# Kernel optimization log

Measured on AMD Instinct MI355X. Metric: run time of the kernel, lower is better.

## Reference

```python
import jax, jax.numpy as jnp
import numpy as np

N_CHAINS = 4
CHAIN_LEN = 512
N = N_CHAINS * CHAIN_LEN          # 2048 residues
H = 128                           # h_channels
FC = 3                            # frame_channels
CIN = H + FC                      # fused sphere channels (131)
NH = 8                            # attention heads
VD = H // 4                       # attn value channels per head
NCOEF = 4                         # lmax=1 -> (lmax+1)^2 coefficients
KNN_K = 30
LR_K = 10
NEG = jnp.float32(-1e30)

BB_IDEAL = np.array([[-0.525, 1.363, 0.0], [0.0, 0.0, 0.0], [1.526, 0.0, 0.0]], np.float32)  # N, CA, C ideal coords


def _safe_norm(v, keepdims=False):
    return jnp.sqrt(jnp.sum(v * v, axis=-1, keepdims=keepdims) + 1e-12)


def _normalize(v):
    return v / _safe_norm(v, keepdims=True)


def _edge_rot_mat(vec):
    # deterministic orthonormal frame with first row along the edge direction
    x = _normalize(vec)
    ref = jnp.where(jnp.abs(x[..., :1]) > 0.99,
                    jnp.array([0.0, 1.0, 0.0], x.dtype),
                    jnp.array([1.0, 0.0, 0.0], x.dtype))
    z = _normalize(jnp.cross(x, ref))
    y = jnp.cross(z, x)
    return jnp.stack([x, y, z], axis=-2)          # [E,3,3]


def _rbf(d, d_min=0.0, d_max=20.0, n=16):
    mu = jnp.linspace(d_min, d_max, n)
    sigma = (d_max - d_min) / n
    return jnp.exp(-(((d[..., None] - mu) / sigma) ** 2))


def _relpos(edge_index, n=16):
    d = (edge_index[0] - edge_index[1]).astype(jnp.float32)
    freq = jnp.exp(jnp.arange(0, n, 2, dtype=jnp.float32) * (-np.log(10000.0) / n))
    ang = d[:, None] * freq
    return jnp.concatenate([jnp.cos(ang), jnp.sin(ang)], axis=-1)


def _quat_to_rot(q):
    w, x, y, z = q[..., 0], q[..., 1], q[..., 2], q[..., 3]
    r0 = jnp.stack([1 - 2 * (y * y + z * z), 2 * (x * y - w * z), 2 * (x * z + w * y)], -1)
    r1 = jnp.stack([2 * (x * y + w * z), 1 - 2 * (x * x + z * z), 2 * (y * z - w * x)], -1)
    r2 = jnp.stack([2 * (x * z - w * y), 2 * (y * z + w * x), 1 - 2 * (x * x + y * y)], -1)
    return jnp.stack([r0, r1, r2], -2)


def _build_edges(trans, batch, seq_local_edge_index):
    d2 = jnp.sum((trans[:, None] - trans[None]) ** 2, -1)   # [N,N]
    same = batch[:, None] == batch[None]
    eye = jnp.eye(N, dtype=bool)
    d2m = jnp.where(same & ~eye, d2, jnp.float32(1e30))
    _, knn_idx = jax.lax.top_k(-d2m, KNN_K)                 # kNN neighbors
    g = jax.random.gumbel(jax.random.key(42), d2m.shape)
    _, lr_idx = jax.lax.top_k(-1.5 * jnp.log(d2m) + g, LR_K)  # inv-cubic sampling p ~ d^-3
    src = jnp.concatenate([knn_idx.reshape(-1), lr_idx.reshape(-1), seq_local_edge_index[0]])
    dst = jnp.concatenate([jnp.repeat(jnp.arange(N), KNN_K), jnp.repeat(jnp.arange(N), LR_K), seq_local_edge_index[1]])
    return jnp.stack([src, dst])


def _forward(rots, trans, node_features, Wa1, ba1, Wa2, Wv, Wo, Wg, Wf1, Wf2, Wr1, br1, Wr2, br2, Wr3, br3, Wt, batch, x_mask, noising_mask, seq_local_edge_index):
    edge_index = _build_edges(trans, batch, seq_local_edge_index)
    src, dst = edge_index[0], edge_index[1]
    vec = trans[src] - trans[dst]
    dist = _safe_norm(vec)
    valid = jnp.isfinite(dist) & (dist > 1e-3)              # edge_select mask (kept static-shape)
    R = _edge_rot_mat(vec)                                  # [E,3,3] per-edge Wigner (l=1)
    ef = jnp.concatenate([_rbf(dist), _relpos(edge_index)], -1)  # [E,32]
    # fuse node embedding with backbone frame atoms and editability flag
    bb_atoms = jnp.einsum('nij,aj->nai', rots, jnp.asarray(BB_IDEAL)) + trans[:, None]  # [N,3atoms,3]
    fused = jnp.zeros((N, NCOEF, CIN), node_features.dtype)
    fused = fused.at[:, :, :H].set(node_features)
    fused = fused.at[:, 1:4, H:].set(jnp.swapaxes(bb_atoms, -1, -2))
    editable = noising_mask & (~x_mask)
    fused = fused.at[:, 0, -1].set(editable.astype(fused.dtype))
    # SO3-equivariant attention (TransBlockV2)
    x0 = fused[:, 0]                                        # invariant l=0 features [N,CIN]
    a_in = jnp.concatenate([x0[src], x0[dst], ef], -1)      # [E, 2*CIN+32]
    logits = jax.nn.leaky_relu(a_in @ Wa1 + ba1) @ Wa2      # [E,NH]
    logits = jnp.where(valid[:, None], logits, NEG)
    m = jax.ops.segment_max(logits, dst, num_segments=N)
    m = jnp.where(m > NEG / 2, m, 0.0)
    p = jnp.where(valid[:, None], jnp.exp(logits - m[dst]), 0.0)
    z = jax.ops.segment_sum(p, dst, num_segments=N)
    attn = p / (z[dst] + 1e-9)                              # segment softmax over incoming edges
    xs = fused[src]
    xs = xs.at[:, 1:4].set(jnp.einsum('eij,ejc->eic', R, xs[:, 1:4]))  # rotate l=1 into edge frame
    v = (xs @ Wv).reshape(xs.shape[0], NCOEF, NH, VD)
    msg = (attn[:, None, :, None] * v).reshape(xs.shape[0], NCOEF, NH * VD)
    msg = msg.at[:, 1:4].set(jnp.einsum('eji,ejc->eic', R, msg[:, 1:4]))  # rotate back (R^T)
    agg = jax.ops.segment_sum(msg, dst, num_segments=N)     # [N,4,NH*VD]
    out = agg @ Wo                                          # [N,4,H]
    # gated equivariant FFN
    y0 = out[:, 0]
    gate = jax.nn.sigmoid(y0 @ Wg)
    f0 = jax.nn.relu(y0 @ Wf1) @ Wf2
    bb_update = jnp.concatenate([(y0 + f0)[:, None], out[:, 1:4] * gate[:, None, :]], axis=1)
    # frame rotation update from invariants
    inv = bb_update[:, 0]
    h1 = jax.nn.relu(inv @ Wr1 + br1)
    h2 = jax.nn.relu(h1 @ Wr2 + br2)
    qv = (h2 @ Wr3 + br3)[:, :3]
    quat = jnp.concatenate([jnp.ones_like(qv[:, :1]), qv], -1)
    quat = quat / jnp.linalg.norm(quat, axis=-1, keepdims=True)
    rot_update = _quat_to_rot(quat)
    # equivariant translation update (SO3_LinearV2 on l=1)
    trans_update = (bb_update[:, 1:4] @ Wt)[..., 0]         # [N,3]
    rots_new = jnp.where(noising_mask[:, None, None], jnp.einsum('nij,njk->nik', rots, rot_update), rots)
    trans_new = jnp.where(noising_mask[:, None], trans + trans_update, trans)
    return rots_new, trans_new, bb_update


def setup_inputs():
    key = jax.random.key(0)
    ks = jax.random.split(key, 20)
    q = jax.random.normal(ks[0], (N, 4))
    q = q / jnp.linalg.norm(q, axis=-1, keepdims=True)
    rots = _quat_to_rot(q)                                  # proper rotation matrices
    trans = jax.random.normal(ks[1], (N, 3)) * 10.0
    node_features = jax.random.normal(ks[2], (N, NCOEF, H)) * 0.1
    batch = jnp.repeat(jnp.arange(N_CHAINS), CHAIN_LEN)
    x_mask = jax.random.bernoulli(ks[3], 0.1, (N,))
    noising_mask = jax.random.bernoulli(ks[4], 0.5, (N,))
    idx = jnp.arange(N)
    nxt = jnp.where((idx + 1) % CHAIN_LEN == 0, idx, idx + 1)
    seq_local_edge_index = jnp.stack([jnp.concatenate([idx, nxt]), jnp.concatenate([nxt, idx])])

    def lin(k, i, o):
        return jax.random.normal(k, (i, o)) / np.sqrt(i)

    AIN = 2 * CIN + 32
    return dict(
        rots=rots, trans=trans, node_features=node_features,
        Wa1=lin(ks[5], AIN, H), ba1=jnp.zeros((H,)),
        Wa2=lin(ks[6], H, NH),
        Wv=lin(ks[7], CIN, NH * VD),
        Wo=lin(ks[8], NH * VD, H),
        Wg=lin(ks[9], H, H), Wf1=lin(ks[10], H, H), Wf2=lin(ks[11], H, H),
        Wr1=lin(ks[12], H, 2 * H), br1=jnp.zeros((2 * H,)),
        Wr2=lin(ks[13], 2 * H, H), br2=jnp.zeros((H,)),
        Wr3=lin(ks[14], H, 6), br3=jnp.zeros((6,)),
        Wt=lin(ks[15], H, 1),
        batch=batch, x_mask=x_mask, noising_mask=noising_mask,
        seq_local_edge_index=seq_local_edge_index)


def reference(rots, trans, node_features, Wa1, ba1, Wa2, Wv, Wo, Wg, Wf1, Wf2, Wr1, br1, Wr2, br2, Wr3, br3, Wt, batch, x_mask, noising_mask, seq_local_edge_index):
    return _forward(rots, trans, node_features, Wa1, ba1, Wa2, Wv, Wo, Wg, Wf1, Wf2, Wr1, br1, Wr2, br2, Wr3, br3, Wt, batch, x_mask, noising_mask, seq_local_edge_index)
```

## Files before the change

kernel.cpp:

```cpp
#include <hip/hip_runtime.h>
#include <hip/hip_bf16.h>
#include <math.h>

#define NN 2048
#define CHAIN 512
#define KNN 30
#define LRK 10
#define NFIX 40
#define NSLOT 42
#define HPAD 132

#define OUT_ROT 0
#define OUT_TRANS (NN*9)
#define OUT_BB (NN*9 + NN*3)

#define THREEFRY_PARTITIONABLE 1

__device__ __forceinline__ int xcd_swz(int b){ return ((b & 7) << 8) | (b >> 3); }

__device__ __forceinline__ unsigned rotl32(unsigned x, unsigned r){ return (x<<r)|(x>>(32u-r)); }

__device__ __forceinline__ void tf_block(unsigned &x0, unsigned &x1){
  const unsigned k0 = 0u, k1 = 42u, k2 = 0x1BD11BDAu ^ 0u ^ 42u;
  x0 += k0; x1 += k1;
#define TFR(a) x0 += x1; x1 = rotl32(x1,(a)); x1 ^= x0;
  TFR(13) TFR(15) TFR(26) TFR(6)   x0 += k1; x1 += k2 + 1u;
  TFR(17) TFR(29) TFR(16) TFR(24)  x0 += k2; x1 += k0 + 2u;
  TFR(13) TFR(15) TFR(26) TFR(6)   x0 += k0; x1 += k1 + 3u;
  TFR(17) TFR(29) TFR(16) TFR(24)  x0 += k1; x1 += k2 + 4u;
  TFR(13) TFR(15) TFR(26) TFR(6)   x0 += k2; x1 += k0 + 5u;
#undef TFR
}

__device__ __forceinline__ float gumbel_from_bits(unsigned bits){
  float f = __uint_as_float((bits >> 9) | 0x3f800000u) - 1.0f;
  const float tiny = 1.17549435e-38f;
  float u = fmaxf(tiny, f * (1.0f - tiny) + tiny);
  return -logf(-logf(u));
}

__device__ __forceinline__ float gumbel_at(unsigned p){
#if THREEFRY_PARTITIONABLE
  unsigned x0 = 0u, x1 = p;
  tf_block(x0, x1);
  return gumbel_from_bits(x0 ^ x1);
#else
  const unsigned HALF = (NN*(unsigned)NN)/2u;
  unsigned c0, c1; bool lo = p < HALF;
  if(lo){ c0 = p; c1 = p + HALF; } else { c0 = p - HALF; c1 = p; }
  tf_block(c0, c1);
  return gumbel_from_bits(lo ? c0 : c1);
#endif
}

__global__ __launch_bounds__(256) void k_prep(
    const float* __restrict__ rots, const float* __restrict__ trans,
    const float* __restrict__ nf, const float* __restrict__ Wa1,
    const float* __restrict__ Wv, const int* __restrict__ xmask,
    const int* __restrict__ nmask,
    float* __restrict__ P, float* __restrict__ U, float* __restrict__ V)
{
  __shared__ __align__(16) float fr[4][4][132];
  int n0 = blockIdx.x*4, t = threadIdx.x;
  for(int i=t; i<2048; i+=256){
    int nd = i>>9, c = (i>>7)&3, kk = i&127;
    fr[nd][c][kk] = nf[(n0+nd)*512 + c*128 + kk];
  }
  if(t < 4){
    fr[t][0][128] = 0.0f; fr[t][0][129] = 0.0f;
    fr[t][0][130] = (nmask[n0+t] != 0 && xmask[n0+t] == 0) ? 1.0f : 0.0f;
  } else if(t >= 16 && t < 52){
    int q = t - 16; int nd = q/9, r = q%9, a = r/3, i = r%3;
    int n = n0 + nd;
    const float BB[3][3] = {{-0.525f,1.363f,0.0f},{0.f,0.f,0.f},{1.526f,0.f,0.f}};
    float bb = rots[n*9+i*3+0]*BB[a][0] + rots[n*9+i*3+1]*BB[a][1]
             + rots[n*9+i*3+2]*BB[a][2] + trans[n*3+i];
    fr[nd][1+i][128+a] = bb;
  }
  __syncthreads();

  float a[4][4];
#pragma unroll
  for(int nd=0;nd<4;nd++)
#pragma unroll
    for(int c=0;c<4;c++) a[nd][c]=0.f;
  for(int j=0;j<128;j+=4){
    float w0=Wv[(j+0)*256+t], w1=Wv[(j+1)*256+t], w2=Wv[(j+2)*256+t], w3=Wv[(j+3)*256+t];
#pragma unroll
    for(int nd=0;nd<4;nd++){
#pragma unroll
      for(int c=0;c<4;c++){
        float4 f4 = *(const float4*)&fr[nd][c][j];
        a[nd][c] += f4.x*w0 + f4.y*w1 + f4.z*w2 + f4.w*w3;
      }
    }
  }
  for(int j=128;j<131;j++){
    float w = Wv[j*256+t];
#pragma unroll
    for(int nd=0;nd<4;nd++)
#pragma unroll
      for(int c=0;c<4;c++) a[nd][c] += fr[nd][c][j]*w;
  }
#pragma unroll
  for(int nd=0;nd<4;nd++)
#pragma unroll
    for(int c=0;c<4;c++) P[(n0+nd)*1024 + c*256 + t] = a[nd][c];

  int k = t & 127;
  int isV = t >> 7;
  const float* Wcol = Wa1 + (isV ? 131*128 : 0);
  float u[4] = {0.f,0.f,0.f,0.f};
  for(int j=0;j<128;j+=4){
    float w0=Wcol[(j+0)*128+k], w1=Wcol[(j+1)*128+k], w2=Wcol[(j+2)*128+k], w3=Wcol[(j+3)*128+k];
#pragma unroll
    for(int nd=0;nd<4;nd++){
      float4 f4 = *(const float4*)&fr[nd][0][j];
      u[nd] += f4.x*w0 + f4.y*w1 + f4.z*w2 + f4.w*w3;
    }
  }
  for(int j=128;j<131;j++){
    float w = Wcol[j*128+k];
#pragma unroll
    for(int nd=0;nd<4;nd++) u[nd] += fr[nd][0][j]*w;
  }
  float* OUT = isV ? V : U;
#pragma unroll
  for(int nd=0;nd<4;nd++) OUT[(n0+nd)*128 + k] = u[nd];
}

__global__ __launch_bounds__(128) void k_topk2(
    const float* __restrict__ trans, int* __restrict__ srcs)
{
  __shared__ unsigned s_kk[CHAIN];
  __shared__ unsigned s_lk[CHAIN];
  int i = blockIdx.x, t = threadIdx.x;
  int base = (i >> 9) << 9;
  float tx = trans[i*3+0], ty = trans[i*3+1], tz = trans[i*3+2];
  for(int q=t; q<CHAIN; q+=128){
    int j = base + q;
    float dx = __fsub_rn(trans[j*3+0], tx);
    float dy = __fsub_rn(trans[j*3+1], ty);
    float dz = __fsub_rn(trans[j*3+2], tz);
    float d2 = __fadd_rn(__fadd_rn(__fmul_rn(dx,dx),__fmul_rn(dy,dy)),__fmul_rn(dz,dz));
    bool val = (j != i);
    float dm = val ? d2 : 1e30f;
    s_kk[q] = __float_as_uint(dm) ^ 0x80000000u;
    if(val){
      float g = gumbel_at((unsigned)(i*NN + j));
      float sc = __fadd_rn(__fmul_rn(-1.5f, logf(dm)), g);
      unsigned b = __float_as_uint(sc);
      unsigned ord = b ^ ((b & 0x80000000u) ? 0xFFFFFFFFu : 0x80000000u);
      s_lk[q] = ~ord;
    } else {
      s_lk[q] = 0xFFFFFFFFu;
    }
  }
  __syncthreads();

  int w = t >> 6, lane = t & 63;
  unsigned* arr = w ? s_lk : s_kk;
  int K = w ? LRK : KNN;
  int outoff = w ? KNN : 0;

  unsigned long long best = ~0ull;
  for(int q=lane; q<CHAIN; q+=64){
    unsigned long long kk = ((unsigned long long)arr[q]<<32) | (unsigned)q;
    if(kk < best) best = kk;
  }
  for(int k=0;k<K;k++){
    unsigned long long r = best;
    for(int off=32; off; off>>=1){
      unsigned long long o = __shfl_xor(r, off, 64);
      if(o < r) r = o;
    }
    int winq = (int)(unsigned)(r & 0xffffffffull);
    if(lane == 0){
      srcs[i*NFIX + outoff + k] = base + winq;
      arr[winq] = 0xFFFFFFFFu;
    }
    asm volatile("s_waitcnt lgkmcnt(0)" ::: "memory");
    __builtin_amdgcn_wave_barrier();
    if((winq & 63) == lane){
      best = ~0ull;
      for(int q=lane; q<CHAIN; q+=64){
        unsigned long long kk = ((unsigned long long)arr[q]<<32) | (unsigned)q;
        if(kk < best) best = kk;
      }
    }
  }
}

__global__ __launch_bounds__(256) void k_attn(
    const float* __restrict__ trans, const float* __restrict__ Wa1,
    const float* __restrict__ ba1, const float* __restrict__ Wa2,
    const float* __restrict__ Wo,
    const float* __restrict__ U, const float* __restrict__ V,
    const float* __restrict__ P,
    const int* __restrict__ srcs, float* __restrict__ Y)
{
  __shared__ int   s_src[NSLOT];
  __shared__ int   s_val[NSLOT];
  __shared__ float s_dist[NSLOT];
  __shared__ float s_rel[NSLOT];
  __shared__ __align__(16) float s_ef[NSLOT*32];
  __shared__ __align__(16) float s_H[NSLOT*HPAD];
  __shared__ __align__(16) float s_wa2t[8*HPAD];
  __shared__ float s_att[NSLOT*8];
  __shared__ __align__(16) float s_agg[4][256];

  int b = blockIdx.x, t = threadIdx.x;
  int d = xcd_swz(b);
  int wave = t >> 6, lane = t & 63;
  int pos = d & (CHAIN-1);

  if(t < NSLOT){
    int src;
    if(t < NFIX)      src = srcs[d*NFIX + t];
    else if(t == NFIX) src = (pos > 0)       ? d-1 : d;
    else               src = (pos < CHAIN-1) ? d+1 : d;
    s_src[t] = src;
    float dx = trans[src*3+0]-trans[d*3+0];
    float dy = trans[src*3+1]-trans[d*3+1];
    float dz = trans[src*3+2]-trans[d*3+2];
    float dist = sqrtf(dx*dx + dy*dy + dz*dz + 1e-12f);
    s_dist[t] = dist;
    s_rel[t] = (float)(src - d);
    s_val[t] = (dist > 1e-3f) ? 1 : 0;
  }
  for(int i=t; i<1024; i+=256){
    int k = i >> 3, h = i & 7;
    s_wa2t[h*HPAD + k] = Wa2[i];
  }

  float wreg0[32], wreg1[32];
#pragma unroll
  for(int f=0; f<32; f++){
    wreg0[f] = Wa1[(262+f)*128 + lane];
    wreg1[f] = Wa1[(262+f)*128 + 64 + lane];
  }
  __syncthreads();

  for(int i=t; i<NSLOT*32; i+=256){
    int e = i >> 5, f = i & 31;
    float v;
    if(f < 16){
      float zz = (s_dist[e] - (float)f * (20.0f/15.0f)) * 0.8f;
      v = expf(-(zz*zz));
    } else {
      int idx = f - 16; int j = idx & 7;
      float fr = expf((float)(2*j) * (float)(-0.5756462732485115));
      float ang = s_rel[e] * fr;
      v = (idx < 8) ? cosf(ang) : sinf(ang);
    }
    s_ef[i] = v;
  }
  __syncthreads();

  {
    float vb0 = V[d*128 + lane], vb1 = V[d*128 + 64 + lane];
    float bb0 = ba1[lane], bb1 = ba1[64 + lane];
    for(int e = wave; e < NSLOT; e += 4){
      int src = s_src[e];
      float h0 = bb0 + vb0 + U[src*128 + lane];
      float h1 = bb1 + vb1 + U[src*128 + 64 + lane];
      const float4* efp = (const float4*)(s_ef + e*32);
#pragma unroll
      for(int q=0; q<8; q++){
        float4 ev = efp[q];
        h0 += ev.x*wreg0[4*q+0] + ev.y*wreg0[4*q+1] + ev.z*wreg0[4*q+2] + ev.w*wreg0[4*q+3];
        h1 += ev.x*wreg1[4*q+0] + ev.y*wreg1[4*q+1] + ev.z*wreg1[4*q+2] + ev.w*wreg1[4*q+3];
      }
      h0 = (h0 >= 0.0f) ? h0 : 0.01f*h0;
      h1 = (h1 >= 0.0f) ? h1 : 0.01f*h1;
      s_H[e*HPAD + lane] = h0;
      s_H[e*HPAD + 64 + lane] = h1;
    }
  }
  __syncthreads();

  for(int p = t; p < NSLOT*8; p += 256){
    int e = p >> 3, h = p & 7;
    const float4* Hp = (const float4*)(s_H + e*HPAD);
    const float4* Wp = (const float4*)(s_wa2t + h*HPAD);
    float acc = 0.f;
#pragma unroll
    for(int q=0; q<32; q++){
      float4 a = Hp[q], w = Wp[q];
      acc += a.x*w.x + a.y*w.y + a.z*w.z + a.w*w.w;
    }
    s_att[p] = s_val[e] ? acc : -1e30f;
  }
  __syncthreads();

  if(t < 64){
    int h = t & 7, g = t >> 3;
    float m = -INFINITY;
    for(int e=g; e<NSLOT; e+=8) m = fmaxf(m, s_att[e*8+h]);
    for(int off=8; off<64; off<<=1) m = fmaxf(m, __shfl_xor(m, off, 64));
    m = (m > -5e29f) ? m : 0.0f;
    float z = 0.0f;
    for(int e=g; e<NSLOT; e+=8){
      float p = expf(s_att[e*8+h] - m);
      s_att[e*8+h] = p; z += p;
    }
    for(int off=8; off<64; off<<=1) z += __shfl_xor(z, off, 64);
    float den = z + 1e-9f;
    for(int e=g; e<NSLOT; e+=8) s_att[e*8+h] = s_att[e*8+h] / den;
  }
  __syncthreads();

  {
    float a0=0.f,a1=0.f,a2=0.f,a3=0.f; int h = t >> 5;
    for(int e=0;e<NSLOT;e++){
      float w = s_att[e*8 + h];
      const float* Pr = P + s_src[e]*1024 + t;
      a0 += w*Pr[0]; a1 += w*Pr[256]; a2 += w*Pr[512]; a3 += w*Pr[768];
    }
    s_agg[0][t]=a0; s_agg[1][t]=a1; s_agg[2][t]=a2; s_agg[3][t]=a3;
  }
  __syncthreads();

  {
    int k = t & 127, cp = (t >> 7) * 2;
    float x0=0.f, x1=0.f;
    for(int u=0; u<256; u+=4){
      float w0=Wo[(u+0)*128+k], w1=Wo[(u+1)*128+k], w2=Wo[(u+2)*128+k], w3=Wo[(u+3)*128+k];
      float4 g0 = *(const float4*)&s_agg[cp][u];
      float4 g1 = *(const float4*)&s_agg[cp+1][u];
      x0 += g0.x*w0 + g0.y*w1 + g0.z*w2 + g0.w*w3;
      x1 += g1.x*w0 + g1.y*w1 + g1.z*w2 + g1.w*w3;
    }
    Y[d*512 + cp*128 + k]     = x0;
    Y[d*512 + (cp+1)*128 + k] = x1;
  }
}

__global__ __launch_bounds__(256) void k_node(
    const float* __restrict__ rots, const float* __restrict__ trans,
    const float* __restrict__ Y,
    const float* __restrict__ Wg, const float* __restrict__ Wf1,
    const float* __restrict__ Wf2, const float* __restrict__ Wr1,
    const float* __restrict__ br1, const float* __restrict__ Wr2,
    const float* __restrict__ br2, const float* __restrict__ Wr3,
    const float* __restrict__ br3, const float* __restrict__ Wt,
    const int* __restrict__ nmask, float* __restrict__ out)
{
  __shared__ __align__(16) float s_y[4][4][128];
  __shared__ __align__(16) float s_t1[4][128];
  __shared__ __align__(16) float s_bb0[4][128];
  __shared__ __align__(16) float s_gv[4][3][128];
  __shared__ __align__(16) float s_h1[4][256];
  __shared__ __align__(16) float s_h2[4][128];
  __shared__ float s_sc[4][8];

  int b = blockIdx.x, t = threadIdx.x;
  int half = t >> 7, k = t & 127;
  int nb = half*2;
  int dbase = b*4;
  for(int i=t; i<4*512; i+=256){
    int nd = i>>9, c=(i>>7)&3, kk=i&127;
    s_y[nd][c][kk] = Y[(dbase+nd)*512 + c*128 + kk];
  }
  __syncthreads();

  float g[2]={0.f,0.f}, f1[2]={0.f,0.f};
  for(int j=0;j<128;j+=4){
    float wg0=Wg[(j+0)*128+k], wg1=Wg[(j+1)*128+k], wg2=Wg[(j+2)*128+k], wg3=Wg[(j+3)*128+k];
    float wf0=Wf1[(j+0)*128+k], wf1_=Wf1[(j+1)*128+k], wf2_=Wf1[(j+2)*128+k], wf3=Wf1[(j+3)*128+k];
#pragma unroll
    for(int nn=0;nn<2;nn++){
      float4 yv = *(const float4*)&s_y[nb+nn][0][j];
      g[nn]  += yv.x*wg0 + yv.y*wg1 + yv.z*wg2 + yv.w*wg3;
      f1[nn] += yv.x*wf0 + yv.y*wf1_ + yv.z*wf2_ + yv.w*wf3;
    }
  }
  float gate[2];
#pragma unroll
  for(int nn=0;nn<2;nn++){
    gate[nn] = 1.0f/(1.0f + expf(-g[nn]));
    s_t1[nb+nn][k] = fmaxf(f1[nn], 0.0f);
  }
  __syncthreads();

  float f0[2]={0.f,0.f};
  for(int j=0;j<128;j+=4){
    float w0=Wf2[(j+0)*128+k], w1=Wf2[(j+1)*128+k], w2=Wf2[(j+2)*128+k], w3=Wf2[(j+3)*128+k];
#pragma unroll
    for(int nn=0;nn<2;nn++){
      float4 tv = *(const float4*)&s_t1[nb+nn][j];
      f0[nn] += tv.x*w0 + tv.y*w1 + tv.z*w2 + tv.w*w3;
    }
  }
#pragma unroll
  for(int nn=0;nn<2;nn++){
    int d = dbase + nb + nn;
    float bb0 = s_y[nb+nn][0][k] + f0[nn];
    s_bb0[nb+nn][k] = bb0;
    out[OUT_BB + d*512 + k] = bb0;
#pragma unroll
    for(int c=1;c<4;c++){
      float v = s_y[nb+nn][c][k] * gate[nn];
      s_gv[nb+nn][c-1][k] = v;
      out[OUT_BB + d*512 + c*128 + k] = v;
    }
  }
  __syncthreads();

  float a1[2], a2[2];
  a1[0]=a1[1]=br1[k]; a2[0]=a2[1]=br1[128+k];
  for(int j=0;j<128;j+=4){
    float w10=Wr1[(j+0)*256+k],     w11=Wr1[(j+1)*256+k],     w12=Wr1[(j+2)*256+k],     w13=Wr1[(j+3)*256+k];
    float w20=Wr1[(j+0)*256+128+k], w21=Wr1[(j+1)*256+128+k], w22=Wr1[(j+2)*256+128+k], w23=Wr1[(j+3)*256+128+k];
#pragma unroll
    for(int nn=0;nn<2;nn++){
      float4 bv = *(const float4*)&s_bb0[nb+nn][j];
      a1[nn] += bv.x*w10 + bv.y*w11 + bv.z*w12 + bv.w*w13;
      a2[nn] += bv.x*w20 + bv.y*w21 + bv.z*w22 + bv.w*w23;
    }
  }
#pragma unroll
  for(int nn=0;nn<2;nn++){
    s_h1[nb+nn][k] = fmaxf(a1[nn], 0.0f);
    s_h1[nb+nn][128+k] = fmaxf(a2[nn], 0.0f);
  }
  __syncthreads();

  float a[2]; a[0]=a[1]=br2[k];
  for(int j=0;j<256;j+=4){
    float w0=Wr2[(j+0)*128+k], w1=Wr2[(j+1)*128+k], w2=Wr2[(j+2)*128+k], w3=Wr2[(j+3)*128+k];
#pragma unroll
    for(int nn=0;nn<2;nn++){
      float4 hv = *(const float4*)&s_h1[nb+nn][j];
      a[nn] += hv.x*w0 + hv.y*w1 + hv.z*w2 + hv.w*w3;
    }
  }
#pragma unroll
  for(int nn=0;nn<2;nn++) s_h2[nb+nn][k] = fmaxf(a[nn], 0.0f);
  __syncthreads();

  if(t < 12){
    int nd = t/3, r = t%3;
    float q = br3[r];
    for(int kk=0;kk<128;kk++) q += s_h2[nd][kk] * Wr3[kk*6 + r];
    s_sc[nd][r] = q;
  } else if(t >= 32 && t < 44){
    int q2 = t-32; int nd = q2/3, i = q2%3;
    float s = 0.f;
    for(int kk=0;kk<128;kk++) s += s_gv[nd][i][kk] * Wt[kk];
    s_sc[nd][4+i] = s;
  }
  __syncthreads();

  if(t < 4){
    int d = dbase + t;
    int nz = nmask[d];
    float q1=s_sc[t][0], q2=s_sc[t][1], q3=s_sc[t][2];
    float nrm = sqrtf(1.0f + q1*q1 + q2*q2 + q3*q3);
    float w=1.0f/nrm, x=q1/nrm, y=q2/nrm, z=q3/nrm;
    float Ru[3][3];
    Ru[0][0]=1.f-2.f*(y*y+z*z); Ru[0][1]=2.f*(x*y-w*z);     Ru[0][2]=2.f*(x*z+w*y);
    Ru[1][0]=2.f*(x*y+w*z);     Ru[1][1]=1.f-2.f*(x*x+z*z); Ru[1][2]=2.f*(y*z-w*x);
    Ru[2][0]=2.f*(x*z-w*y);     Ru[2][1]=2.f*(y*z+w*x);     Ru[2][2]=1.f-2.f*(x*x+y*y);
    for(int i=0;i<3;i++){
      for(int j=0;j<3;j++){
        float rv;
        if(nz){
          rv = rots[d*9+i*3+0]*Ru[0][j] + rots[d*9+i*3+1]*Ru[1][j] + rots[d*9+i*3+2]*Ru[2][j];
        } else {
          rv = rots[d*9+i*3+j];
        }
        out[OUT_ROT + d*9 + i*3 + j] = rv;
      }
      float tv = trans[d*3+i];
      out[OUT_TRANS + d*3 + i] = nz ? (tv + s_sc[t][4+i]) : tv;
    }
  }
}

extern "C" void kernel_launch(void* const* d_in, const int* in_sizes, int n_in,
                              void* d_out, int out_size, void* d_ws, size_t ws_size,
                              hipStream_t stream)
{
  (void)in_sizes; (void)n_in; (void)out_size; (void)ws_size;
  const float* rots = (const float*)d_in[0];
  const float* trans = (const float*)d_in[1];
  const float* nf   = (const float*)d_in[2];
  const float* Wa1  = (const float*)d_in[3];
  const float* ba1  = (const float*)d_in[4];
  const float* Wa2  = (const float*)d_in[5];
  const float* Wv   = (const float*)d_in[6];
  const float* Wo   = (const float*)d_in[7];
  const float* Wg   = (const float*)d_in[8];
  const float* Wf1  = (const float*)d_in[9];
  const float* Wf2  = (const float*)d_in[10];
  const float* Wr1  = (const float*)d_in[11];
  const float* br1  = (const float*)d_in[12];
  const float* Wr2  = (const float*)d_in[13];
  const float* br2  = (const float*)d_in[14];
  const float* Wr3  = (const float*)d_in[15];
  const float* br3  = (const float*)d_in[16];
  const float* Wt   = (const float*)d_in[17];
  const int* xmask  = (const int*)d_in[19];
  const int* nmask  = (const int*)d_in[20];

  float* P = (float*)d_ws;
  float* U = P + NN*1024;
  float* V = U + NN*128;
  int* srcs = (int*)(V + NN*128);
  float* Y  = (float*)(srcs + NN*NFIX);

  k_prep<<<NN/4, 256, 0, stream>>>(rots, trans, nf, Wa1, Wv, xmask, nmask, P, U, V);
  k_topk2<<<NN, 128, 0, stream>>>(trans, srcs);
  k_attn<<<NN, 256, 0, stream>>>(trans, Wa1, ba1, Wa2, Wo, U, V, P, srcs, Y);
  k_node<<<NN/4, 256, 0, stream>>>(rots, trans, Y, Wg, Wf1, Wf2,
                                   Wr1, br1, Wr2, br2, Wr3, br3, Wt,
                                   nmask, (float*)d_out);
}
```

Before: 159.1 us.

## Merge top-k and prep kernels into one launch, shrink attention LDS and vectorize P

Folds the top-k neighbor selection blocks and the per-node projection blocks into one heterogeneous kernel, so the two independent stages run concurrently in a single launch. In the attention kernel, one reused shared buffer replaces the edge-feature, transposed-Wa2 and aggregate buffers, and the per-thread register weights drop from 64 to 32. Together with a launch bound of 5 blocks per CU, this aims to raise occupancy. P is stored and read as float4 in an interleaved layout for wider memory transactions. The cost is an extra barrier in the attention kernel and top-k blocks where only half the threads work during selection.

```diff
diff --git a/kernel.cpp b/kernel.cpp
--- a/kernel.cpp
+++ b/kernel.cpp
@@ -9,6 +9,7 @@
 #define NFIX 40
 #define NSLOT 42
 #define HPAD 132
+#define AGPAD 260
 
 #define OUT_ROT 0
 #define OUT_TRANS (NN*9)
@@ -53,15 +54,80 @@
 #endif
 }
 
-__global__ __launch_bounds__(256) void k_prep(
+__global__ __launch_bounds__(256) void k_pretop(
     const float* __restrict__ rots, const float* __restrict__ trans,
     const float* __restrict__ nf, const float* __restrict__ Wa1,
     const float* __restrict__ Wv, const int* __restrict__ xmask,
     const int* __restrict__ nmask,
-    float* __restrict__ P, float* __restrict__ U, float* __restrict__ V)
+    float* __restrict__ P, float* __restrict__ U, float* __restrict__ V,
+    int* __restrict__ srcs)
 {
-  __shared__ __align__(16) float fr[4][4][132];
-  int n0 = blockIdx.x*4, t = threadIdx.x;
+  __shared__ __align__(16) char smem[4*4*132*4];
+  int bb = blockIdx.x, t = threadIdx.x;
+
+  if(bb < NN){
+    unsigned* s_kk = (unsigned*)smem;
+    unsigned* s_lk = s_kk + CHAIN;
+    int i = bb;
+    int base = (i >> 9) << 9;
+    float tx = trans[i*3+0], ty = trans[i*3+1], tz = trans[i*3+2];
+    for(int q=t; q<CHAIN; q+=256){
+      int j = base + q;
+      float dx = __fsub_rn(trans[j*3+0], tx);
+      float dy = __fsub_rn(trans[j*3+1], ty);
+      float dz = __fsub_rn(trans[j*3+2], tz);
+      float d2 = __fadd_rn(__fadd_rn(__fmul_rn(dx,dx),__fmul_rn(dy,dy)),__fmul_rn(dz,dz));
+      bool val = (j != i);
+      float dm = val ? d2 : 1e30f;
+      s_kk[q] = __float_as_uint(dm) ^ 0x80000000u;
+      if(val){
+        float g = gumbel_at((unsigned)(i*NN + j));
+        float sc = __fadd_rn(__fmul_rn(-1.5f, logf(dm)), g);
+        unsigned b = __float_as_uint(sc);
+        unsigned ord = b ^ ((b & 0x80000000u) ? 0xFFFFFFFFu : 0x80000000u);
+        s_lk[q] = ~ord;
+      } else {
+        s_lk[q] = 0xFFFFFFFFu;
+      }
+    }
+    __syncthreads();
+    if(t < 128){
+      int w = t >> 6, lane = t & 63;
+      unsigned* arr = w ? s_lk : s_kk;
+      int K = w ? LRK : KNN;
+      int outoff = w ? KNN : 0;
+      unsigned long long best = ~0ull;
+      for(int q=lane; q<CHAIN; q+=64){
+        unsigned long long kk = ((unsigned long long)arr[q]<<32) | (unsigned)q;
+        if(kk < best) best = kk;
+      }
+      for(int k=0;k<K;k++){
+        unsigned long long r = best;
+        for(int off=32; off; off>>=1){
+          unsigned long long o = __shfl_xor(r, off, 64);
+          if(o < r) r = o;
+        }
+        int winq = (int)(unsigned)(r & 0xffffffffull);
+        if(lane == 0){
+          srcs[i*NFIX + outoff + k] = base + winq;
+          arr[winq] = 0xFFFFFFFFu;
+        }
+        asm volatile("s_waitcnt lgkmcnt(0)" ::: "memory");
+        __builtin_amdgcn_wave_barrier();
+        if((winq & 63) == lane){
+          best = ~0ull;
+          for(int q=lane; q<CHAIN; q+=64){
+            unsigned long long kk = ((unsigned long long)arr[q]<<32) | (unsigned)q;
+            if(kk < best) best = kk;
+          }
+        }
+      }
+    }
+    return;
+  }
+
+  float (*fr)[4][132] = (float (*)[4][132])smem;
+  int n0 = (bb - NN)*4;
   for(int i=t; i<2048; i+=256){
     int nd = i>>9, c = (i>>7)&3, kk = i&127;
     fr[nd][c][kk] = nf[(n0+nd)*512 + c*128 + kk];
@@ -73,9 +139,9 @@
     int q = t - 16; int nd = q/9, r = q%9, a = r/3, i = r%3;
     int n = n0 + nd;
     const float BB[3][3] = {{-0.525f,1.363f,0.0f},{0.f,0.f,0.f},{1.526f,0.f,0.f}};
-    float bb = rots[n*9+i*3+0]*BB[a][0] + rots[n*9+i*3+1]*BB[a][1]
-             + rots[n*9+i*3+2]*BB[a][2] + trans[n*3+i];
-    fr[nd][1+i][128+a] = bb;
+    float bb_ = rots[n*9+i*3+0]*BB[a][0] + rots[n*9+i*3+1]*BB[a][1]
+              + rots[n*9+i*3+2]*BB[a][2] + trans[n*3+i];
+    fr[nd][1+i][128+a] = bb_;
   }
   __syncthreads();
 
@@ -103,9 +169,10 @@
       for(int c=0;c<4;c++) a[nd][c] += fr[nd][c][j]*w;
   }
 #pragma unroll
-  for(int nd=0;nd<4;nd++)
-#pragma unroll
-    for(int c=0;c<4;c++) P[(n0+nd)*1024 + c*256 + t] = a[nd][c];
+  for(int nd=0;nd<4;nd++){
+    float4 v4; v4.x=a[nd][0]; v4.y=a[nd][1]; v4.z=a[nd][2]; v4.w=a[nd][3];
+    *(float4*)&P[(n0+nd)*1024 + t*4] = v4;
+  }
 
   int k = t & 127;
   int isV = t >> 7;
@@ -129,69 +196,7 @@
   for(int nd=0;nd<4;nd++) OUT[(n0+nd)*128 + k] = u[nd];
 }
 
-__global__ __launch_bounds__(128) void k_topk2(
-    const float* __restrict__ trans, int* __restrict__ srcs)
-{
-  __shared__ unsigned s_kk[CHAIN];
-  __shared__ unsigned s_lk[CHAIN];
-  int i = blockIdx.x, t = threadIdx.x;
-  int base = (i >> 9) << 9;
-  float tx = trans[i*3+0], ty = trans[i*3+1], tz = trans[i*3+2];
-  for(int q=t; q<CHAIN; q+=128){
-    int j = base + q;
-    float dx = __fsub_rn(trans[j*3+0], tx);
-    float dy = __fsub_rn(trans[j*3+1], ty);
-    float dz = __fsub_rn(trans[j*3+2], tz);
-    float d2 = __fadd_rn(__fadd_rn(__fmul_rn(dx,dx),__fmul_rn(dy,dy)),__fmul_rn(dz,dz));
-    bool val = (j != i);
-    float dm = val ? d2 : 1e30f;
-    s_kk[q] = __float_as_uint(dm) ^ 0x80000000u;
-    if(val){
-      float g = gumbel_at((unsigned)(i*NN + j));
-      float sc = __fadd_rn(__fmul_rn(-1.5f, logf(dm)), g);
-      unsigned b = __float_as_uint(sc);
-      unsigned ord = b ^ ((b & 0x80000000u) ? 0xFFFFFFFFu : 0x80000000u);
-      s_lk[q] = ~ord;
-    } else {
-      s_lk[q] = 0xFFFFFFFFu;
-    }
-  }
-  __syncthreads();
-
-  int w = t >> 6, lane = t & 63;
-  unsigned* arr = w ? s_lk : s_kk;
-  int K = w ? LRK : KNN;
-  int outoff = w ? KNN : 0;
-
-  unsigned long long best = ~0ull;
-  for(int q=lane; q<CHAIN; q+=64){
-    unsigned long long kk = ((unsigned long long)arr[q]<<32) | (unsigned)q;
-    if(kk < best) best = kk;
-  }
-  for(int k=0;k<K;k++){
-    unsigned long long r = best;
-    for(int off=32; off; off>>=1){
-      unsigned long long o = __shfl_xor(r, off, 64);
-      if(o < r) r = o;
-    }
-    int winq = (int)(unsigned)(r & 0xffffffffull);
-    if(lane == 0){
-      srcs[i*NFIX + outoff + k] = base + winq;
-      arr[winq] = 0xFFFFFFFFu;
-    }
-    asm volatile("s_waitcnt lgkmcnt(0)" ::: "memory");
-    __builtin_amdgcn_wave_barrier();
-    if((winq & 63) == lane){
-      best = ~0ull;
-      for(int q=lane; q<CHAIN; q+=64){
-        unsigned long long kk = ((unsigned long long)arr[q]<<32) | (unsigned)q;
-        if(kk < best) best = kk;
-      }
-    }
-  }
-}
-
-__global__ __launch_bounds__(256) void k_attn(
+__global__ __launch_bounds__(256, 5) void k_attn(
     const float* __restrict__ trans, const float* __restrict__ Wa1,
     const float* __restrict__ ba1, const float* __restrict__ Wa2,
     const float* __restrict__ Wo,
@@ -203,16 +208,14 @@
   __shared__ int   s_val[NSLOT];
   __shared__ float s_dist[NSLOT];
   __shared__ float s_rel[NSLOT];
-  __shared__ __align__(16) float s_ef[NSLOT*32];
   __shared__ __align__(16) float s_H[NSLOT*HPAD];
-  __shared__ __align__(16) float s_wa2t[8*HPAD];
+  __shared__ __align__(16) float s_mux[NSLOT*32];
   __shared__ float s_att[NSLOT*8];
-  __shared__ __align__(16) float s_agg[4][256];
 
   int b = blockIdx.x, t = threadIdx.x;
   int d = xcd_swz(b);
-  int wave = t >> 6, lane = t & 63;
   int pos = d & (CHAIN-1);
+  int k = t & 127, grp = t >> 7;
 
   if(t < NSLOT){
     int src;
@@ -228,17 +231,11 @@
     s_rel[t] = (float)(src - d);
     s_val[t] = (dist > 1e-3f) ? 1 : 0;
   }
-  for(int i=t; i<1024; i+=256){
-    int k = i >> 3, h = i & 7;
-    s_wa2t[h*HPAD + k] = Wa2[i];
-  }
-
-  float wreg0[32], wreg1[32];
-#pragma unroll
-  for(int f=0; f<32; f++){
-    wreg0[f] = Wa1[(262+f)*128 + lane];
-    wreg1[f] = Wa1[(262+f)*128 + 64 + lane];
-  }
+
+  float wreg[32];
+#pragma unroll
+  for(int f=0; f<32; f++) wreg[f] = Wa1[(262+f)*128 + k];
+  float ubias = ba1[k] + V[d*128 + k];
   __syncthreads();
 
   for(int i=t; i<NSLOT*32; i+=256){
@@ -253,36 +250,33 @@
       float ang = s_rel[e] * fr;
       v = (idx < 8) ? cosf(ang) : sinf(ang);
     }
-    s_ef[i] = v;
-  }
-  __syncthreads();
-
-  {
-    float vb0 = V[d*128 + lane], vb1 = V[d*128 + 64 + lane];
-    float bb0 = ba1[lane], bb1 = ba1[64 + lane];
-    for(int e = wave; e < NSLOT; e += 4){
-      int src = s_src[e];
-      float h0 = bb0 + vb0 + U[src*128 + lane];
-      float h1 = bb1 + vb1 + U[src*128 + 64 + lane];
-      const float4* efp = (const float4*)(s_ef + e*32);
-#pragma unroll
-      for(int q=0; q<8; q++){
-        float4 ev = efp[q];
-        h0 += ev.x*wreg0[4*q+0] + ev.y*wreg0[4*q+1] + ev.z*wreg0[4*q+2] + ev.w*wreg0[4*q+3];
-        h1 += ev.x*wreg1[4*q+0] + ev.y*wreg1[4*q+1] + ev.z*wreg1[4*q+2] + ev.w*wreg1[4*q+3];
-      }
-      h0 = (h0 >= 0.0f) ? h0 : 0.01f*h0;
-      h1 = (h1 >= 0.0f) ? h1 : 0.01f*h1;
-      s_H[e*HPAD + lane] = h0;
-      s_H[e*HPAD + 64 + lane] = h1;
-    }
+    s_mux[i] = v;
+  }
+  __syncthreads();
+
+  for(int e = grp; e < NSLOT; e += 2){
+    float h = ubias + U[s_src[e]*128 + k];
+    const float4* efp = (const float4*)(s_mux + e*32);
+#pragma unroll
+    for(int q=0; q<8; q++){
+      float4 ev = efp[q];
+      h += ev.x*wreg[4*q+0] + ev.y*wreg[4*q+1] + ev.z*wreg[4*q+2] + ev.w*wreg[4*q+3];
+    }
+    h = (h >= 0.0f) ? h : 0.01f*h;
+    s_H[e*HPAD + k] = h;
+  }
+  __syncthreads();
+
+  for(int i=t; i<1024; i+=256){
+    int kk = i >> 3, h = i & 7;
+    s_mux[h*HPAD + kk] = Wa2[i];
   }
   __syncthreads();
 
   for(int p = t; p < NSLOT*8; p += 256){
     int e = p >> 3, h = p & 7;
     const float4* Hp = (const float4*)(s_H + e*HPAD);
-    const float4* Wp = (const float4*)(s_wa2t + h*HPAD);
+    const float4* Wp = (const float4*)(s_mux + h*HPAD);
     float acc = 0.f;
 #pragma unroll
     for(int q=0; q<32; q++){
@@ -311,25 +305,31 @@
   __syncthreads();
 
   {
-    float a0=0.f,a1=0.f,a2=0.f,a3=0.f; int h = t >> 5;
+    int h = t >> 5;
+    float a0=0.f,a1=0.f,a2=0.f,a3=0.f;
     for(int e=0;e<NSLOT;e++){
       float w = s_att[e*8 + h];
-      const float* Pr = P + s_src[e]*1024 + t;
-      a0 += w*Pr[0]; a1 += w*Pr[256]; a2 += w*Pr[512]; a3 += w*Pr[768];
-    }
-    s_agg[0][t]=a0; s_agg[1][t]=a1; s_agg[2][t]=a2; s_agg[3][t]=a3;
+      float4 p4 = *(const float4*)(P + s_src[e]*1024 + t*4);
+      a0 += w*p4.x; a1 += w*p4.y; a2 += w*p4.z; a3 += w*p4.w;
+    }
+    s_mux[0*AGPAD + t] = a0;
+    s_mux[1*AGPAD + t] = a1;
+    s_mux[2*AGPAD + t] = a2;
+    s_mux[3*AGPAD + t] = a3;
   }
   __syncthreads();
 
   {
-    int k = t & 127, cp = (t >> 7) * 2;
+    int cp = grp*2;
+    const float* g0 = s_mux + cp*AGPAD;
+    const float* g1 = s_mux + (cp+1)*AGPAD;
     float x0=0.f, x1=0.f;
     for(int u=0; u<256; u+=4){
       float w0=Wo[(u+0)*128+k], w1=Wo[(u+1)*128+k], w2=Wo[(u+2)*128+k], w3=Wo[(u+3)*128+k];
-      float4 g0 = *(const float4*)&s_agg[cp][u];
-      float4 g1 = *(const float4*)&s_agg[cp+1][u];
-      x0 += g0.x*w0 + g0.y*w1 + g0.z*w2 + g0.w*w3;
-      x1 += g1.x*w0 + g1.y*w1 + g1.z*w2 + g1.w*w3;
+      float4 a0 = *(const float4*)(g0 + u);
+      float4 a1 = *(const float4*)(g1 + u);
+      x0 += a0.x*w0 + a0.y*w1 + a0.z*w2 + a0.w*w3;
+      x1 += a1.x*w0 + a1.y*w1 + a1.z*w2 + a1.w*w3;
     }
     Y[d*512 + cp*128 + k]     = x0;
     Y[d*512 + (cp+1)*128 + k] = x1;
@@ -510,8 +510,8 @@
   int* srcs = (int*)(V + NN*128);
   float* Y  = (float*)(srcs + NN*NFIX);
 
-  k_prep<<<NN/4, 256, 0, stream>>>(rots, trans, nf, Wa1, Wv, xmask, nmask, P, U, V);
-  k_topk2<<<NN, 128, 0, stream>>>(trans, srcs);
+  k_pretop<<<NN + NN/4, 256, 0, stream>>>(rots, trans, nf, Wa1, Wv, xmask, nmask,
+                                          P, U, V, srcs);
   k_attn<<<NN, 256, 0, stream>>>(trans, Wa1, ba1, Wa2, Wo, U, V, P, srcs, Y);
   k_node<<<NN/4, 256, 0, stream>>>(rots, trans, Y, Wg, Wf1, Wf2,
                                    Wr1, br1, Wr2, br2, Wr3, br3, Wt,
```

After: 237.8 us. 1.49x slower.
